# Optimization experiments

Hardware: AMD Instinct MI355X
Metric: run time of the kernel (lower is better)

## Reference

```python
import jax, jax.numpy as jnp
import numpy as np

EPSILON = 0.1


def setup_inputs() -> dict:
    key = jax.random.key(0)
    ks = jax.random.split(key, 6)
    N, E, F_IN, F_OUT, NF = 50000, 800000, 256, 96, 3
    x = jax.random.normal(ks[0], (N, F_IN), dtype=jnp.float32)
    adj_vals = jax.random.uniform(ks[1], (E,), dtype=jnp.float32)
    d_scales = jax.random.uniform(ks[2], (NF, N), dtype=jnp.float32)
    # xavier-uniform-ish weights
    limit = np.sqrt(6.0 / (F_IN + F_OUT)).astype(np.float32)
    weights = jax.random.uniform(ks[3], (NF, F_IN, F_OUT), dtype=jnp.float32,
                                 minval=-limit, maxval=limit)
    bias = jnp.zeros((F_OUT,), dtype=jnp.float32)
    edge_index = jax.random.randint(ks[4], (2, E), 0, N, dtype=jnp.int32)
    return {"x": x, "adj_vals": adj_vals, "d_scales": d_scales,
            "weights": weights, "bias": bias, "edge_index": edge_index}


def reference(x, adj_vals, d_scales, weights, bias, edge_index):
    N = x.shape[0]
    row, col = edge_index[0], edge_index[1]

    # degree with self loops (add_remaining_self_loops adds 1 per node)
    deg = jax.ops.segment_sum(jnp.ones_like(adj_vals), row, num_segments=N) + 1.0
    eps_deg_inv = EPSILON / deg  # [N], diagonal of sparse_degree(..., epsilon)

    def spmm(t):  # symadj @ t via edge list
        return jax.ops.segment_sum(adj_vals[:, None] * t[col], row, num_segments=N)

    out = jnp.zeros((N, weights.shape[2]), dtype=x.dtype)
    n_filters = weights.shape[0]
    for ii in range(n_filters):
        sign = -1.0 if ii == 0 else 1.0  # Ad = symadj -/+ eps*diag(deg^-1)
        t = d_scales[ii][:, None] * (x @ weights[ii])          # D @ (x W)
        t = spmm(t) + sign * eps_deg_inv[:, None] * t          # Ad @ t
        t = d_scales[ii][:, None] * jax.nn.relu(t)             # D @ relu(t)
        out = out + t
    return out + bias
```

## Files before the change

kernel.cpp:

```cpp
#include <hip/hip_runtime.h>

#define EPSILON 0.1f
#define F_IN 256
#define F_OUT 96
#define NF 3
#define TCOLS 288
#define TSTRIDE 320
#define CAP 64
#define BN 96
#define CW 104
#define NCVT (TCOLS * F_IN / 4)

#define RPB 64
#define NBINS 782
#define BCAP 1536
#define EPB 4096

typedef __attribute__((ext_vector_type(8))) short bf8_t;
typedef __attribute__((ext_vector_type(4))) float f32x4;

__device__ inline ushort f2b(float f) {
    union { float f; unsigned u; } v; v.f = f;
    unsigned u = v.u;
    return (ushort)((u + 0x7FFFu + ((u >> 16) & 1u)) >> 16);
}
__device__ inline float blo(unsigned u) { return __uint_as_float(u << 16); }
__device__ inline float bhi(unsigned u) { return __uint_as_float(u & 0xffff0000u); }

__device__ inline bf8_t cvt8(float4 a, float4 b) {
    bf8_t r;
    r[0] = (short)f2b(a.x); r[1] = (short)f2b(a.y);
    r[2] = (short)f2b(a.z); r[3] = (short)f2b(a.w);
    r[4] = (short)f2b(b.x); r[5] = (short)f2b(b.y);
    r[6] = (short)f2b(b.z); r[7] = (short)f2b(b.w);
    return r;
}

__global__ __launch_bounds__(256) void setup_kernel(const float* __restrict__ w,
                                                    ushort* __restrict__ wt,
                                                    int* __restrict__ gcur) {
    int tid = blockIdx.x * 256 + threadIdx.x;
    if (tid < NCVT) {
        int base = tid * 4;
        int gc = base >> 8;
        int k  = base & 255;
        int ii = gc / F_OUT;
        int c  = gc - ii * F_OUT;
        const float* wp = w + (size_t)ii * (F_IN * F_OUT) + (size_t)k * F_OUT + c;
        ushort4 o;
        o.x = f2b(wp[0 * F_OUT]);
        o.y = f2b(wp[1 * F_OUT]);
        o.z = f2b(wp[2 * F_OUT]);
        o.w = f2b(wp[3 * F_OUT]);
        *(ushort4*)(wt + base) = o;
    } else {
        int z = (tid - NCVT) * 4;
        if (z + 3 < NBINS) {
            *(int4*)(gcur + z) = make_int4(0, 0, 0, 0);
        } else {
            for (int j = z; j < NBINS && j >= 0; ++j) gcur[j] = 0;
        }
    }
}

__global__ __launch_bounds__(256) void bin_cvt_kernel(
        const int* __restrict__ row, const int* __restrict__ col,
        const float* __restrict__ vals, int E,
        int* __restrict__ gcur, int2* __restrict__ gout,
        const float* __restrict__ x, ushort* __restrict__ xb, int N, int nbin) {
    __shared__ int2 ord[EPB];
    __shared__ int hist[NBINS];
    __shared__ int gbase[NBINS];
    __shared__ int basex[NBINS];
    __shared__ int ts[512];

    if ((int)blockIdx.x < nbin) {
        int tid = threadIdx.x;
        for (int i = tid; i < NBINS; i += 256) hist[i] = 0;
        __syncthreads();

        int e0 = (int)blockIdx.x * EPB;
        int4 r4[4], c4[4]; float4 v4[4];
        int rank[16], binv[16], valv[16];
        unsigned recx[16];
        #pragma unroll
        for (int g = 0; g < 4; ++g) {
            int e = e0 + tid * 4 + g * 1024;
            if (e + 3 < E) {
                r4[g] = *(const int4*)(row + e);
                c4[g] = *(const int4*)(col + e);
                v4[g] = *(const float4*)(vals + e);
            } else {
                int4 rr, cc; float4 vv;
                int* rp = (int*)&rr; int* cp = (int*)&cc; float* vp = (float*)&vv;
                #pragma unroll
                for (int j = 0; j < 4; ++j) {
                    int ee = e + j;
                    rp[j] = (ee < E) ? row[ee] : -1;
                    cp[j] = (ee < E) ? col[ee] : 0;
                    vp[j] = (ee < E) ? vals[ee] : 0.f;
                }
                r4[g] = rr; c4[g] = cc; v4[g] = vv;
            }
        }
        #pragma unroll
        for (int g = 0; g < 4; ++g) {
            const int* rp = (const int*)&r4[g];
            const int* cp = (const int*)&c4[g];
            const float* vp = (const float*)&v4[g];
            #pragma unroll
            for (int j = 0; j < 4; ++j) {
                int s = g * 4 + j;
                int r = rp[j];
                if (r >= 0) {
                    int b = r >> 6;
                    binv[s] = b;
                    recx[s] = (unsigned)(cp[j] & 0xffff) |
                              ((unsigned)(r & 63) << 16) | ((unsigned)b << 22);
                    valv[s] = __float_as_int(vp[j]);
                    rank[s] = atomicAdd(&hist[b], 1);
                } else {
                    binv[s] = -1; rank[s] = 0; recx[s] = 0; valv[s] = 0;
                }
            }
        }
        __syncthreads();

        int b0 = tid * 4;
        int h0 = (b0     < NBINS) ? hist[b0]     : 0;
        int h1 = (b0 + 1 < NBINS) ? hist[b0 + 1] : 0;
        int h2 = (b0 + 2 < NBINS) ? hist[b0 + 2] : 0;
        int h3 = (b0 + 3 < NBINS) ? hist[b0 + 3] : 0;
        int tot = h0 + h1 + h2 + h3;
        ts[tid] = tot;
        __syncthreads();
        int src = 0;
        #pragma unroll
        for (int off = 1; off < 256; off <<= 1) {
            int v = ts[src * 256 + tid];
            if (tid >= off) v += ts[src * 256 + tid - off];
            ts[(src ^ 1) * 256 + tid] = v;
            __syncthreads();
            src ^= 1;
        }
        int excl = ts[src * 256 + tid] - tot;
        if (b0     < NBINS) basex[b0]     = excl;
        if (b0 + 1 < NBINS) basex[b0 + 1] = excl + h0;
        if (b0 + 2 < NBINS) basex[b0 + 2] = excl + h0 + h1;
        if (b0 + 3 < NBINS) basex[b0 + 3] = excl + h0 + h1 + h2;
        #pragma unroll
        for (int q = 0; q < 4; ++q) {
            int i = b0 + q;
            if (i < NBINS) {
                int h = hist[i];
                gbase[i] = h ? atomicAdd(&gcur[i], h) : 0;
            }
        }
        __syncthreads();

        #pragma unroll
        for (int s = 0; s < 16; ++s)
            if (binv[s] >= 0)
                ord[basex[binv[s]] + rank[s]] = make_int2((int)recx[s], valv[s]);
        __syncthreads();

        int total = ts[src * 256 + 255];
        for (int i = tid; i < total; i += 256) {
            int2 rec = ord[i];
            int b = ((unsigned)rec.x) >> 22;
            int pos = gbase[b] + (i - basex[b]);
            if (pos < BCAP)
                gout[(size_t)b * BCAP + pos] = rec;
        }
    } else {
        size_t base = ((size_t)((int)blockIdx.x - nbin) * 256 + threadIdx.x) * 8;
        if (base < (size_t)N * F_IN) {
            float4 a = *(const float4*)(x + base);
            float4 b = *(const float4*)(x + base + 4);
            bf8_t o = cvt8(a, b);
            *(bf8_t*)(xb + base) = o;
        }
    }
}

__global__ __launch_bounds__(512) void gemm_bucket(
        const ushort* __restrict__ xb, const ushort* __restrict__ wt,
        const float* __restrict__ dsc, ushort* __restrict__ t, int N,
        int nper, int nw,
        const int2* __restrict__ gout, const int* __restrict__ gcur,
        int* __restrict__ cnt, int2* __restrict__ evs2) {
    __shared__ ushort Bs[BN * F_IN];

    int tid = threadIdx.x;

    if ((int)blockIdx.x < NBINS) {
        int2* buck = (int2*)Bs;
        int*  lcnt = (int*)(Bs + 16384);
        int b = blockIdx.x;
        if (tid < RPB) lcnt[tid] = 0;
        __syncthreads();

        int nrec = gcur[b];
        if (nrec > BCAP) nrec = BCAP;
        for (int i = tid; i < nrec; i += 512) {
            int2 rec = gout[(size_t)b * BCAP + i];
            int rl = (rec.x >> 16) & 63;
            int c  = rec.x & 0xffff;
            int k = atomicAdd(&lcnt[rl], 1);
            if (k < CAP) buck[rl * CAP + k] = make_int2(c * TSTRIDE, rec.y);
        }
        __syncthreads();

        int row0 = b * RPB;
        if (tid < RPB && row0 + tid < N) cnt[row0 + tid] = lcnt[tid];

        int lane = tid & 63, wave = tid >> 6;
        for (int r = wave; r < RPB; r += 8) {
            int rowg = row0 + r;
            if (rowg >= N) break;
            int m = min(lcnt[r], CAP);
            if (lane < m)
                evs2[(size_t)rowg * CAP + lane] = buck[r * CAP + lane];
        }
        return;
    }

    int lb = (int)blockIdx.x - NBINS;
    int xcd = lb & 7, li = lb >> 3;
    int w = xcd * nper + li;
    if (w >= nw) return;
    int mb = w / 3, cb = w - mb * 3;

    int lane = tid & 63, wave = tid >> 6;
    int cl = lane & 15, quad = lane >> 4;
    int gc0 = cb * BN;
    int m0 = mb * 128 + wave * 16;
    int mrow = m0 + cl;
    bool aok = (mrow < N);

    #pragma unroll
    for (int i = 0; i < 6; ++i) {
        int F = tid + i * 512;
        int rem = F & 63;
        int q = rem >> 4, c = rem & 15;
        int ksj = F >> 6;
        int ks = ksj / 6, j = ksj - ks * 6;
        int gc = gc0 + j * 16 + c;
        *(uint4*)(Bs + (size_t)F * 8) =
            *(const uint4*)(wt + (size_t)gc * F_IN + ks * 32 + q * 8);
    }

    uint4 areg[8];
    const ushort* xp = xb + (size_t)mrow * F_IN + quad * 8;
    const uint4 zu = make_uint4(0, 0, 0, 0);
    #pragma unroll
    for (int ks = 0; ks < 8; ++ks)
        areg[ks] = aok ? *(const uint4*)(xp + ks * 32) : zu;

    f32x4 acc[6];
    #pragma unroll
    for (int j = 0; j < 6; ++j) acc[j] = (f32x4){0.f, 0.f, 0.f, 0.f};

    __syncthreads();

    #pragma unroll
    for (int ks = 0; ks < 8; ++ks) {
        bf8_t a = *(const bf8_t*)&areg[ks];
        const ushort* bb = Bs + ((size_t)(ks * 6) * 64 + lane) * 8;
        #pragma unroll
        for (int j = 0; j < 6; ++j) {
            bf8_t b = *(const bf8_t*)(bb + j * 64 * 8);
            acc[j] = __builtin_amdgcn_mfma_f32_16x16x32_bf16(a, b, acc[j], 0, 0, 0);
        }
    }

    __syncthreads();
    ushort* Cw = Bs + wave * (16 * CW);
    float dscv[3][4];
    #pragma unroll
    for (int ii = 0; ii < 3; ++ii)
        #pragma unroll
        for (int r = 0; r < 4; ++r) {
            int rowg = m0 + quad * 4 + r;
            dscv[ii][r] = (rowg < N) ? dsc[(size_t)ii * N + rowg] : 0.f;
        }
    #pragma unroll
    for (int j = 0; j < 6; ++j) {
        int ii = (gc0 + j * 16) / F_OUT;
        #pragma unroll
        for (int r = 0; r < 4; ++r)
            Cw[(quad * 4 + r) * CW + j * 16 + cl] = f2b(dscv[ii][r] * acc[j][r]);
    }
    #pragma unroll
    for (int it = 0; it < 3; ++it) {
        int idx = lane + it * 64;
        int r = idx / 12, ch = idx - r * 12;
        int grow = m0 + r;
        if (grow < N)
            *(uint4*)(t + (size_t)grow * TSTRIDE + gc0 + ch * 8) =
                *(const uint4*)&Cw[r * CW + ch * 8];
    }
}

__device__ inline void acc8(float* acc, uint4 a, float v) {
    acc[0] = fmaf(v, blo(a.x), acc[0]); acc[1] = fmaf(v, bhi(a.x), acc[1]);
    acc[2] = fmaf(v, blo(a.y), acc[2]); acc[3] = fmaf(v, bhi(a.y), acc[3]);
    acc[4] = fmaf(v, blo(a.z), acc[4]); acc[5] = fmaf(v, bhi(a.z), acc[5]);
    acc[6] = fmaf(v, blo(a.w), acc[6]); acc[7] = fmaf(v, bhi(a.w), acc[7]);
}

__global__ __launch_bounds__(256) void spmm_kernel(const ushort* __restrict__ t,
                                                   const int2* __restrict__ evs2,
                                                   const int* __restrict__ cnt,
                                                   const float* __restrict__ dsc,
                                                   const float* __restrict__ bias,
                                                   float* __restrict__ out, int N) {
    int lane = threadIdx.x & 63;
    int wave = threadIdx.x >> 6;
    int n = blockIdx.x * 4 + wave;
    if (n >= N) return;

    int deg = cnt[n];
    int mm = (deg < CAP) ? deg : CAP;
    int s = n * CAP, e = s + mm;
    int coff = (lane < 40) ? lane * 8 : 0;

    float acc[8];
    #pragma unroll
    for (int j = 0; j < 8; ++j) acc[j] = 0.f;

    for (int base = s; base < e; base += 64) {
        int idx = base + lane;
        int2 q = make_int2(0, 0);
        if (idx < e) q = evs2[idx];
        int m = min(64, e - base);
        int j = 0;
        for (; j + 3 < m; j += 4) {
            int c0 = __shfl(q.x, j, 64);
            int c1 = __shfl(q.x, j + 1, 64);
            int c2 = __shfl(q.x, j + 2, 64);
            int c3 = __shfl(q.x, j + 3, 64);
            float v0 = __int_as_float(__shfl(q.y, j, 64));
            float v1 = __int_as_float(__shfl(q.y, j + 1, 64));
            float v2 = __int_as_float(__shfl(q.y, j + 2, 64));
            float v3 = __int_as_float(__shfl(q.y, j + 3, 64));
            uint4 a0 = *(const uint4*)(t + (size_t)c0 + coff);
            uint4 a1 = *(const uint4*)(t + (size_t)c1 + coff);
            uint4 a2 = *(const uint4*)(t + (size_t)c2 + coff);
            uint4 a3 = *(const uint4*)(t + (size_t)c3 + coff);
            acc8(acc, a0, v0);
            acc8(acc, a1, v1);
            acc8(acc, a2, v2);
            acc8(acc, a3, v3);
        }
        for (; j < m; ++j) {
            int c = __shfl(q.x, j, 64);
            float v = __int_as_float(__shfl(q.y, j, 64));
            uint4 a = *(const uint4*)(t + (size_t)c + coff);
            acc8(acc, a, v);
        }
    }

    float sign = (lane < 12) ? -1.f : 1.f;
    float epsdi = EPSILON / (float)(deg + 1);
    int ii = lane / 12;
    float dscv = (lane < 36) ? dsc[(size_t)ii * N + n] : 0.f;
    uint4 sv = *(const uint4*)(t + (size_t)n * TSTRIDE + coff);
    float se = sign * epsdi;
    float val[8];
    {
        unsigned u;
        u = sv.x; val[0] = fmaf(se, blo(u), acc[0]); val[1] = fmaf(se, bhi(u), acc[1]);
        u = sv.y; val[2] = fmaf(se, blo(u), acc[2]); val[3] = fmaf(se, bhi(u), acc[3]);
        u = sv.z; val[4] = fmaf(se, blo(u), acc[4]); val[5] = fmaf(se, bhi(u), acc[5]);
        u = sv.w; val[6] = fmaf(se, blo(u), acc[6]); val[7] = fmaf(se, bhi(u), acc[7]);
    }
    #pragma unroll
    for (int j = 0; j < 8; ++j) val[j] = fmaxf(val[j], 0.f) * dscv;

    float res[8];
    #pragma unroll
    for (int j = 0; j < 8; ++j) {
        float r1 = __shfl(val[j], lane + 12, 64);
        float r2 = __shfl(val[j], lane + 24, 64);
        res[j] = val[j] + r1 + r2;
    }
    if (lane < 12) {
        float4 b0 = *(const float4*)(bias + lane * 8);
        float4 b1 = *(const float4*)(bias + lane * 8 + 4);
        float4 o0 = make_float4(res[0] + b0.x, res[1] + b0.y, res[2] + b0.z, res[3] + b0.w);
        float4 o1 = make_float4(res[4] + b1.x, res[5] + b1.y, res[6] + b1.z, res[7] + b1.w);
        *(float4*)(out + (size_t)n * F_OUT + lane * 8) = o0;
        *(float4*)(out + (size_t)n * F_OUT + lane * 8 + 4) = o1;
    }
}

extern "C" void kernel_launch(void* const* d_in, const int* in_sizes, int n_in,
                              void* d_out, int out_size, void* d_ws, size_t ws_size,
                              hipStream_t stream) {
    const float* x    = (const float*)d_in[0];
    const float* adj  = (const float*)d_in[1];
    const float* dsc  = (const float*)d_in[2];
    const float* w    = (const float*)d_in[3];
    const float* bias = (const float*)d_in[4];
    const int*   ei   = (const int*)d_in[5];

    int E = in_sizes[1];
    int N = in_sizes[0] / F_IN;
    const int* row = ei;
    const int* col = ei + E;
    float* out = (float*)d_out;

    char* p = (char*)d_ws;
    auto take = [&](size_t bytes) {
        char* r = p;
        p += (bytes + 255) & ~(size_t)255;
        return r;
    };
    int*    cnt  = (int*)take((size_t)N * 4);
    int2*   evs2 = (int2*)take((size_t)N * CAP * 8);
    ushort* wt   = (ushort*)take((size_t)TCOLS * F_IN * 2);
    ushort* xb   = (ushort*)take((size_t)N * F_IN * 2);
    ushort* t    = (ushort*)take(((size_t)N * TSTRIDE + 256) * 2);
    int*    gcur = (int*)take((size_t)NBINS * 4);
    int2*   gout = (int2*)take((size_t)NBINS * BCAP * 8);

    int nzero = (NBINS + 3) / 4;
    setup_kernel<<<(NCVT + nzero + 255) / 256, 256, 0, stream>>>(w, wt, gcur);

    int nbin  = (E + EPB - 1) / EPB;
    int ncvtx = ((N * F_IN / 8) + 255) / 256;
    bin_cvt_kernel<<<nbin + ncvtx, 256, 0, stream>>>(row, col, adj, E, gcur, gout,
                                                     x, xb, N, nbin);

    int nt = (N + 127) / 128;
    int nw = 3 * nt;
    int nper = (((nw + 7) / 8) + 2) / 3 * 3;
    gemm_bucket<<<NBINS + 8 * nper, 512, 0, stream>>>(xb, wt, dsc, t, N, nper, nw,
                                                      gout, gcur, cnt, evs2);
    spmm_kernel<<<(N + 3) / 4, 256, 0, stream>>>(t, evs2, cnt, dsc, bias, out, N);
}
```

Measured before the change: 220.5 us.

## Drop local sort in edge binning, pad global bin counters, halve edges per block

The binning kernel no longer sorts edges into shared memory with a prefix scan before writing. Each edge is now written straight to its global bucket slot, computed from the block's atomic base plus the edge's local rank. Global bin counters are padded to one per 128-byte line to reduce atomic contention, and each block now handles half as many edges. This removes several barriers and the scan, but the global writes become scattered instead of coalesced, and there are twice as many blocks issuing atomics.

```diff
diff --git a/kernel.cpp b/kernel.cpp
--- a/kernel.cpp
+++ b/kernel.cpp
@@ -14,7 +14,8 @@
 #define RPB 64
 #define NBINS 782
 #define BCAP 1536
-#define EPB 4096
+#define EPB 2048
+#define GPAD 32
 
 typedef __attribute__((ext_vector_type(8))) short bf8_t;
 typedef __attribute__((ext_vector_type(4))) float f32x4;
@@ -55,10 +56,8 @@
         *(ushort4*)(wt + base) = o;
     } else {
         int z = (tid - NCVT) * 4;
-        if (z + 3 < NBINS) {
+        if (z + 3 < NBINS * GPAD) {
             *(int4*)(gcur + z) = make_int4(0, 0, 0, 0);
-        } else {
-            for (int j = z; j < NBINS && j >= 0; ++j) gcur[j] = 0;
         }
     }
 }
@@ -68,11 +67,8 @@
         const float* __restrict__ vals, int E,
         int* __restrict__ gcur, int2* __restrict__ gout,
         const float* __restrict__ x, ushort* __restrict__ xb, int N, int nbin) {
-    __shared__ int2 ord[EPB];
     __shared__ int hist[NBINS];
     __shared__ int gbase[NBINS];
-    __shared__ int basex[NBINS];
-    __shared__ int ts[512];
 
     if ((int)blockIdx.x < nbin) {
         int tid = threadIdx.x;
@@ -80,11 +76,11 @@
         __syncthreads();
 
         int e0 = (int)blockIdx.x * EPB;
-        int4 r4[4], c4[4]; float4 v4[4];
-        int rank[16], binv[16], valv[16];
-        unsigned recx[16];
-        #pragma unroll
-        for (int g = 0; g < 4; ++g) {
+        int4 r4[2], c4[2]; float4 v4[2];
+        int rank[8], binv[8], valv[8];
+        unsigned recx[8];
+        #pragma unroll
+        for (int g = 0; g < 2; ++g) {
             int e = e0 + tid * 4 + g * 1024;
             if (e + 3 < E) {
                 r4[g] = *(const int4*)(row + e);
@@ -104,7 +100,7 @@
             }
         }
         #pragma unroll
-        for (int g = 0; g < 4; ++g) {
+        for (int g = 0; g < 2; ++g) {
             const int* rp = (const int*)&r4[g];
             const int* cp = (const int*)&c4[g];
             const float* vp = (const float*)&v4[g];
@@ -126,51 +122,24 @@
         }
         __syncthreads();
 
-        int b0 = tid * 4;
-        int h0 = (b0     < NBINS) ? hist[b0]     : 0;
-        int h1 = (b0 + 1 < NBINS) ? hist[b0 + 1] : 0;
-        int h2 = (b0 + 2 < NBINS) ? hist[b0 + 2] : 0;
-        int h3 = (b0 + 3 < NBINS) ? hist[b0 + 3] : 0;
-        int tot = h0 + h1 + h2 + h3;
-        ts[tid] = tot;
-        __syncthreads();
-        int src = 0;
-        #pragma unroll
-        for (int off = 1; off < 256; off <<= 1) {
-            int v = ts[src * 256 + tid];
-            if (tid >= off) v += ts[src * 256 + tid - off];
-            ts[(src ^ 1) * 256 + tid] = v;
-            __syncthreads();
-            src ^= 1;
-        }
-        int excl = ts[src * 256 + tid] - tot;
-        if (b0     < NBINS) basex[b0]     = excl;
-        if (b0 + 1 < NBINS) basex[b0 + 1] = excl + h0;
-        if (b0 + 2 < NBINS) basex[b0 + 2] = excl + h0 + h1;
-        if (b0 + 3 < NBINS) basex[b0 + 3] = excl + h0 + h1 + h2;
         #pragma unroll
         for (int q = 0; q < 4; ++q) {
-            int i = b0 + q;
+            int i = threadIdx.x * 4 + q;
             if (i < NBINS) {
                 int h = hist[i];
-                gbase[i] = h ? atomicAdd(&gcur[i], h) : 0;
+                gbase[i] = h ? atomicAdd(&gcur[i * GPAD], h) : 0;
             }
         }
         __syncthreads();
 
         #pragma unroll
-        for (int s = 0; s < 16; ++s)
-            if (binv[s] >= 0)
-                ord[basex[binv[s]] + rank[s]] = make_int2((int)recx[s], valv[s]);
-        __syncthreads();
-
-        int total = ts[src * 256 + 255];
-        for (int i = tid; i < total; i += 256) {
-            int2 rec = ord[i];
-            int b = ((unsigned)rec.x) >> 22;
-            int pos = gbase[b] + (i - basex[b]);
-            if (pos < BCAP)
-                gout[(size_t)b * BCAP + pos] = rec;
+        for (int s = 0; s < 8; ++s) {
+            int b = binv[s];
+            if (b >= 0) {
+                int pos = gbase[b] + rank[s];
+                if (pos < BCAP)
+                    gout[(size_t)b * BCAP + pos] = make_int2((int)recx[s], valv[s]);
+            }
         }
     } else {
         size_t base = ((size_t)((int)blockIdx.x - nbin) * 256 + threadIdx.x) * 8;
@@ -200,7 +169,7 @@
         if (tid < RPB) lcnt[tid] = 0;
         __syncthreads();
 
-        int nrec = gcur[b];
+        int nrec = gcur[b * GPAD];
         if (nrec > BCAP) nrec = BCAP;
         for (int i = tid; i < nrec; i += 512) {
             int2 rec = gout[(size_t)b * BCAP + i];
@@ -422,10 +391,10 @@
     ushort* wt   = (ushort*)take((size_t)TCOLS * F_IN * 2);
     ushort* xb   = (ushort*)take((size_t)N * F_IN * 2);
     ushort* t    = (ushort*)take(((size_t)N * TSTRIDE + 256) * 2);
-    int*    gcur = (int*)take((size_t)NBINS * 4);
+    int*    gcur = (int*)take((size_t)NBINS * GPAD * 4);
     int2*   gout = (int2*)take((size_t)NBINS * BCAP * 8);
 
-    int nzero = (NBINS + 3) / 4;
+    int nzero = (NBINS * GPAD + 3) / 4;
     setup_kernel<<<(NCVT + nzero + 255) / 256, 256, 0, stream>>>(w, wt, gcur);
 
     int nbin  = (E + EPB - 1) / EPB;
```

Measured after the change: 220.6 us. About the same (+0.1%).
